# Kernel tuning notes

Measured on AMD Instinct MI355X. Metric: run time of the kernel, lower is better.

The kernel has to match this reference:

```python
import jax, jax.numpy as jnp
import numpy as np

VERTICES = np.array([[-1.0, -1.0, 1.0], [-1.0, 1.0, 1.0], [1.0, 1.0, 1.0], [1.0, -1.0, 1.0]], dtype=np.float32)  # [4,3]


def _gather2d(img, yi, xi):
    # img: [C,IH,IW], yi/xi: [OH,OW] int32 -> [C,OH,OW]
    return img[:, yi, xi]


def _grid_sample_bilinear_zero(inp, grid):
    # inp: [B,C,IH,IW], grid: [B,OH,OW,2] in [-1,1] (x,y), align_corners=True (old torch semantics)
    B, C, IH, IW = inp.shape
    gx = grid[..., 0]
    gy = grid[..., 1]
    ix = (gx + 1.0) * (IW - 1) * 0.5
    iy = (gy + 1.0) * (IH - 1) * 0.5
    x0 = jnp.floor(ix)
    y0 = jnp.floor(iy)
    x1 = x0 + 1.0
    y1 = y0 + 1.0
    wx1 = ix - x0  # frac weights
    wy1 = iy - y0
    wx0 = 1.0 - wx1
    wy0 = 1.0 - wy1

    def corner(xf, yf, w):
        inb = ((xf >= 0) & (xf <= IW - 1) & (yf >= 0) & (yf <= IH - 1)).astype(inp.dtype)
        xi = jnp.clip(xf, 0, IW - 1).astype(jnp.int32)
        yi = jnp.clip(yf, 0, IH - 1).astype(jnp.int32)
        vals = jax.vmap(_gather2d)(inp, yi, xi)  # [B,C,OH,OW]
        return vals * (w * inb)[:, None, :, :]

    out = (corner(x0, y0, wx0 * wy0) + corner(x1, y0, wx1 * wy0)
           + corner(x0, y1, wx0 * wy1) + corner(x1, y1, wx1 * wy1))
    return out


def affine_spatial_transform(inp, theta, OH, OW):
    B, C, IH, IW = inp.shape
    hs = jnp.linspace(-1.0, 1.0, OH)
    ws = jnp.linspace(-1.0, 1.0, OW)
    hh = jnp.broadcast_to(hs[:, None], (OH, OW))
    ww = jnp.broadcast_to(ws[None, :], (OH, OW))
    t = jnp.stack([ww, hh, jnp.ones((OH, OW), dtype=inp.dtype)], axis=2)  # [OH,OW,3]
    # source_grid = theta @ t : [B,OH,OW,2]
    grid = jnp.einsum('bij,hwj->bhwi', theta, t)
    out = _grid_sample_bilinear_zero(inp, grid)
    v = jnp.asarray(VERTICES)  # [4,3]
    vout = jnp.einsum('bij,vj->bvi', theta, v)  # [B,4,2]
    x_coord = (vout[..., 0] + 1.0) * IW * 0.5
    y_coord = (vout[..., 1] + 1.0) * IH * 0.5
    vertices_out = jnp.stack([x_coord, y_coord], axis=2)  # [B,4,2]
    return out, vertices_out


def setup_inputs() -> dict:
    key = jax.random.key(0)
    k1, k2 = jax.random.split(key)
    B, C, IH, IW = 16, 64, 256, 256
    inp = jax.random.normal(k1, (B, C, IH, IW), dtype=jnp.float32)
    theta = jax.random.normal(k2, (B, 2, 3), dtype=jnp.float32)
    return {"input": inp, "theta": theta, "OH": 256, "OW": 256}


def reference(input, theta, OH, OW):
    return affine_spatial_transform(input, theta, OH, OW)
```

## Files before the change

kernel.cpp:

```cpp
#include <hip/hip_runtime.h>

#define B  16
#define C  64
#define IH 256
#define IW 256
#define OH 256
#define OW 256

#define TW 16
#define TH 16
#define NWT (OW / TW)
#define NHT (OH / TH)
#define NB  (B * NHT * NWT)
#define CAP 4096

typedef float f4 __attribute__((ext_vector_type(4)));
typedef float f2 __attribute__((ext_vector_type(2)));
typedef f2 __attribute__((aligned(4))) f2u;

__global__ __launch_bounds__(256) void ast_fused(const float* __restrict__ inp,
                                                 const float* __restrict__ theta,
                                                 float* __restrict__ out) {
    const int tid = threadIdx.x;

    if (blockIdx.x == 0 && tid < B * 4) {
        const int b_ = tid >> 2;
        const int v  = tid & 3;
        const float vx_tab[4] = {-1.0f, -1.0f, 1.0f, 1.0f};
        const float vy_tab[4] = {-1.0f,  1.0f, 1.0f, -1.0f};
        const float Vx = vx_tab[v];
        const float Vy = vy_tab[v];
        const float ox = theta[b_*6+0]*Vx + theta[b_*6+1]*Vy + theta[b_*6+2];
        const float oy = theta[b_*6+3]*Vx + theta[b_*6+4]*Vy + theta[b_*6+5];
        float* vo = out + (size_t)B * C * OH * OW;
        vo[b_*8 + v*2 + 0] = (ox + 1.0f) * ((float)IW * 0.5f);
        vo[b_*8 + v*2 + 1] = (oy + 1.0f) * ((float)IH * 0.5f);
    }

    int id = (int)blockIdx.x;
    id = (id & 7) * (NB >> 3) + (id >> 3);

    const int wt = id & (NWT - 1);
    const int ht = (id >> 4) & (NHT - 1);
    const int b  = id >> 8;

    const int tx = tid & (TW - 1);
    const int ty = tid >> 4;
    const int w = wt * TW + tx;
    const int h = ht * TH + ty;

    const float t00 = theta[b*6+0], t01 = theta[b*6+1], t02 = theta[b*6+2];
    const float t10 = theta[b*6+3], t11 = theta[b*6+4], t12 = theta[b*6+5];

    const float sWn = 2.0f / (float)(OW - 1);
    const float sHn = 2.0f / (float)(OH - 1);

    const float wn = -1.0f + sWn * (float)w;
    const float hn = -1.0f + sHn * (float)h;
    const float ix = (t00 * wn + t01 * hn + t02 + 1.0f) * ((float)(IW - 1) * 0.5f);
    const float iy = (t10 * wn + t11 * hn + t12 + 1.0f) * ((float)(IH - 1) * 0.5f);

    const float x0f = floorf(ix);
    const float y0f = floorf(iy);
    const float wx1 = ix - x0f;
    const float wy1 = iy - y0f;
    const float wx0 = 1.0f - wx1;
    const float wy0 = 1.0f - wy1;

    const bool inx0 = (x0f >= 0.0f) && (x0f <= (float)(IW - 1));
    const bool inx1 = (x0f + 1.0f >= 0.0f) && (x0f + 1.0f <= (float)(IW - 1));
    const bool iny0 = (y0f >= 0.0f) && (y0f <= (float)(IH - 1));
    const bool iny1 = (y0f + 1.0f >= 0.0f) && (y0f + 1.0f <= (float)(IH - 1));

    const float w00 = (inx0 && iny0) ? wx0 * wy0 : 0.0f;
    const float w10 = (inx1 && iny0) ? wx1 * wy0 : 0.0f;
    const float w01 = (inx0 && iny1) ? wx0 * wy1 : 0.0f;
    const float w11 = (inx1 && iny1) ? wx1 * wy1 : 0.0f;

    const float wnA = -1.0f + sWn * (float)(wt * TW);
    const float wnB = -1.0f + sWn * (float)(wt * TW + TW - 1);
    const float hnA = -1.0f + sHn * (float)(ht * TH);
    const float hnB = -1.0f + sHn * (float)(ht * TH + TH - 1);

    const float ixAA = (t00*wnA + t01*hnA + t02 + 1.0f) * 127.5f;
    const float ixAB = (t00*wnA + t01*hnB + t02 + 1.0f) * 127.5f;
    const float ixBA = (t00*wnB + t01*hnA + t02 + 1.0f) * 127.5f;
    const float ixBB = (t00*wnB + t01*hnB + t02 + 1.0f) * 127.5f;
    const float iyAA = (t10*wnA + t11*hnA + t12 + 1.0f) * 127.5f;
    const float iyAB = (t10*wnA + t11*hnB + t12 + 1.0f) * 127.5f;
    const float iyBA = (t10*wnB + t11*hnA + t12 + 1.0f) * 127.5f;
    const float iyBB = (t10*wnB + t11*hnB + t12 + 1.0f) * 127.5f;

    const float min_ix = fminf(fminf(ixAA, ixAB), fminf(ixBA, ixBB));
    const float max_ix = fmaxf(fmaxf(ixAA, ixAB), fmaxf(ixBA, ixBB));
    const float min_iy = fminf(fminf(iyAA, iyAB), fminf(iyBA, iyBB));
    const float max_iy = fmaxf(fmaxf(iyAA, iyAB), fmaxf(iyBA, iyBB));

    float* o = out + ((size_t)(b * C) << 16) + (size_t)(h * OW + w);

    if (max_ix < -1.0f || min_ix > 256.0f || max_iy < -1.0f || min_iy > 256.0f) {
        #pragma unroll 8
        for (int c = 0; c < C; ++c) {
            __builtin_nontemporal_store(0.0f, o);
            o += OH * OW;
        }
        return;
    }

    const int bx0 = min(max((int)floorf(min_ix) - 1, 0), IW - 1);
    const int bx1 = min(max((int)floorf(max_ix) + 2, 0), IW - 1);
    const int by0 = min(max((int)floorf(min_iy) - 1, 0), IH - 1);
    const int by1 = min(max((int)floorf(max_iy) + 2, 0), IH - 1);

    const int Wneed = bx1 - bx0 + 4;
    int lw = 32 - __builtin_clz((unsigned)(Wneed - 1));
    if (lw < 3) lw = 3;
    if (lw > 8) lw = 8;
    const int P   = 1 << lw;
    const int Pp  = P + 4;
    const int ax0p = min(bx0 & ~3, IW - P);
    const int Hd  = by1 - by0 + 1;

    const int x0i = (int)x0f;
    const int y0i = (int)y0f;
    const float* plane = inp + ((size_t)(b * C) << 16);

    if (Hd * Pp > CAP) {
        const int  basex = min(max(x0i, 0), IW - 2);
        const bool sA = (x0i <= IW - 2);
        const bool sB = (x0i >= 0);
        const int  y0c = min(max(y0i,     0), IH - 1);
        const int  y1c = min(max(y0i + 1, 0), IH - 1);
        const int off0 = y0c * IW + basex;
        const int off1 = y1c * IW + basex;
        const float* pl = plane;
        for (int c = 0; c < C; ++c) {
            const f2 ra = *(const f2u*)(pl + off0);
            const f2 rb = *(const f2u*)(pl + off1);
            const float a00 = sA ? ra.x : ra.y;
            const float a10 = sB ? ra.y : ra.x;
            const float b00 = sA ? rb.x : rb.y;
            const float b11 = sB ? rb.y : rb.x;
            float v = w00 * a00;
            v = fmaf(w10, a10, v);
            v = fmaf(w01, b00, v);
            v = fmaf(w11, b11, v);
            __builtin_nontemporal_store(v, o);
            pl += IH * IW;
            o  += OH * OW;
        }
        return;
    }

    const int xin = x0i - ax0p;
    const int rin = y0i - by0;
    const int xc0 = min(max(xin, 0), P - 2);
    const bool selA = (xin <= P - 2);
    const bool selB = (xin >= 0);
    const int r0 = min(max(rin,     0), Hd - 1);
    const int r1 = min(max(rin + 1, 0), Hd - 1);
    const int ad0 = r0 * Pp + xc0;
    const int ad1 = r1 * Pp + xc0;

    const int S = Hd << lw;
    int  gsrc[4];
    int  ldst[4];
    bool act[4];
    #pragma unroll
    for (int g = 0; g < 4; ++g) {
        const int i4 = g * 1024 + (tid << 2);
        act[g] = (i4 < S);
        const int r  = i4 >> lw;
        const int xb = i4 & (P - 1);
        gsrc[g] = (by0 + r) * IW + ax0p + xb;
        ldst[g] = r * Pp + xb;
    }

    __shared__ float sb[2][CAP];

    f4 pf[4];
    #pragma unroll
    for (int g = 0; g < 4; ++g)
        if (act[g]) pf[g] = *(const f4*)(plane + gsrc[g]);

    #pragma unroll 2
    for (int c = 0; c < C; ++c) {
        const int cur = c & 1;
        float* dst = &sb[cur][0];
        #pragma unroll
        for (int g = 0; g < 4; ++g)
            if (act[g]) *(f4*)(dst + ldst[g]) = pf[g];
        if (c + 1 < C) {
            const float* pl = plane + ((size_t)(c + 1) << 16);
            #pragma unroll
            for (int g = 0; g < 4; ++g)
                if (act[g]) pf[g] = *(const f4*)(pl + gsrc[g]);
        }
        __syncthreads();
        const float* Lb = &sb[cur][0];
        const float p00 = Lb[ad0], p01 = Lb[ad0 + 1];
        const float p10 = Lb[ad1], p11 = Lb[ad1 + 1];
        const float a00 = selA ? p00 : p01;
        const float a10 = selB ? p01 : p00;
        const float b00 = selA ? p10 : p11;
        const float b11 = selB ? p11 : p10;
        float v = w00 * a00;
        v = fmaf(w10, a10, v);
        v = fmaf(w01, b00, v);
        v = fmaf(w11, b11, v);
        __builtin_nontemporal_store(v, o);
        o += OH * OW;
    }
}

extern "C" void kernel_launch(void* const* d_in, const int* in_sizes, int n_in,
                              void* d_out, int out_size, void* d_ws, size_t ws_size,
                              hipStream_t stream) {
    const float* inp   = (const float*)d_in[0];
    const float* theta = (const float*)d_in[1];
    float* out = (float*)d_out;

    ast_fused<<<NB, 256, 0, stream>>>(inp, theta, out);
}
```

Before: 579.9 us.

## Shrink LDS tile, deepen channel prefetch pipeline, use lightweight barriers

```diff
diff --git a/kernel.cpp b/kernel.cpp
--- a/kernel.cpp
+++ b/kernel.cpp
@@ -12,15 +12,22 @@
 #define NWT (OW / TW)
 #define NHT (OH / TH)
 #define NB  (B * NHT * NWT)
-#define CAP 4096
+#define CAPU 2048
+#define CAPF (CAPU + 256)
 
 typedef float f4 __attribute__((ext_vector_type(4)));
 typedef float f2 __attribute__((ext_vector_type(2)));
 typedef f2 __attribute__((aligned(4))) f2u;
 
-__global__ __launch_bounds__(256) void ast_fused(const float* __restrict__ inp,
-                                                 const float* __restrict__ theta,
-                                                 float* __restrict__ out) {
+#define BAR() do {                                         \
+    asm volatile("s_waitcnt lgkmcnt(0)" ::: "memory");     \
+    __builtin_amdgcn_s_barrier();                          \
+    asm volatile("" ::: "memory");                         \
+} while (0)
+
+__global__ __launch_bounds__(256, 8) void ast_fused(const float* __restrict__ inp,
+                                                    const float* __restrict__ theta,
+                                                    float* __restrict__ out) {
     const int tid = threadIdx.x;
 
     if (blockIdx.x == 0 && tid < B * 4) {
@@ -116,16 +123,16 @@
     int lw = 32 - __builtin_clz((unsigned)(Wneed - 1));
     if (lw < 3) lw = 3;
     if (lw > 8) lw = 8;
-    const int P   = 1 << lw;
-    const int Pp  = P + 4;
+    const int P    = 1 << lw;
+    const int Pp   = P + 4;
     const int ax0p = min(bx0 & ~3, IW - P);
-    const int Hd  = by1 - by0 + 1;
+    const int Hd   = by1 - by0 + 1;
 
     const int x0i = (int)x0f;
     const int y0i = (int)y0f;
     const float* plane = inp + ((size_t)(b * C) << 16);
 
-    if (Hd * Pp > CAP) {
+    if (Hd * Pp > CAPU) {
         const int  basex = min(max(x0i, 0), IW - 2);
         const bool sA = (x0i <= IW - 2);
         const bool sB = (x0i >= 0);
@@ -163,54 +170,83 @@
     const int ad1 = r1 * Pp + xc0;
 
     const int S = Hd << lw;
-    int  gsrc[4];
-    int  ldst[4];
-    bool act[4];
+    int gsrc[2], ldst[2];
     #pragma unroll
-    for (int g = 0; g < 4; ++g) {
+    for (int g = 0; g < 2; ++g) {
         const int i4 = g * 1024 + (tid << 2);
-        act[g] = (i4 < S);
-        const int r  = i4 >> lw;
-        const int xb = i4 & (P - 1);
-        gsrc[g] = (by0 + r) * IW + ax0p + xb;
-        ldst[g] = r * Pp + xb;
-    }
-
-    __shared__ float sb[2][CAP];
-
-    f4 pf[4];
-    #pragma unroll
-    for (int g = 0; g < 4; ++g)
-        if (act[g]) pf[g] = *(const f4*)(plane + gsrc[g]);
-
-    #pragma unroll 2
-    for (int c = 0; c < C; ++c) {
-        const int cur = c & 1;
-        float* dst = &sb[cur][0];
-        #pragma unroll
-        for (int g = 0; g < 4; ++g)
-            if (act[g]) *(f4*)(dst + ldst[g]) = pf[g];
-        if (c + 1 < C) {
-            const float* pl = plane + ((size_t)(c + 1) << 16);
-            #pragma unroll
-            for (int g = 0; g < 4; ++g)
-                if (act[g]) pf[g] = *(const f4*)(pl + gsrc[g]);
+        if (i4 < S) {
+            const int r  = i4 >> lw;
+            const int xb = i4 & (P - 1);
+            gsrc[g] = (by0 + r) * IW + ax0p + xb;
+            ldst[g] = r * Pp + xb;
+        } else {
+            gsrc[g] = by0 * IW + ax0p;
+            ldst[g] = CAPU + ((tid & 63) << 2);
         }
-        __syncthreads();
-        const float* Lb = &sb[cur][0];
+    }
+
+    __shared__ float sb[2][CAPF];
+    float* const b0 = &sb[0][0];
+    float* const b1 = &sb[1][0];
+
+    auto samp = [&](const float* Lb) -> float {
         const float p00 = Lb[ad0], p01 = Lb[ad0 + 1];
         const float p10 = Lb[ad1], p11 = Lb[ad1 + 1];
         const float a00 = selA ? p00 : p01;
         const float a10 = selB ? p01 : p00;
-        const float b00 = selA ? p10 : p11;
-        const float b11 = selB ? p11 : p10;
+        const float c00 = selA ? p10 : p11;
+        const float c11 = selB ? p11 : p10;
         float v = w00 * a00;
         v = fmaf(w10, a10, v);
-        v = fmaf(w01, b00, v);
-        v = fmaf(w11, b11, v);
-        __builtin_nontemporal_store(v, o);
+        v = fmaf(w01, c00, v);
+        v = fmaf(w11, c11, v);
+        return v;
+    };
+
+    const float* pld = plane;
+    f4 pfA0, pfA1, pfB0, pfB1;
+
+    pfA0 = *(const f4*)(pld + gsrc[0]);
+    pfA1 = *(const f4*)(pld + gsrc[1]);
+    pld += IH * IW;
+    pfB0 = *(const f4*)(pld + gsrc[0]);
+    pfB1 = *(const f4*)(pld + gsrc[1]);
+    pld += IH * IW;
+    *(f4*)(b0 + ldst[0]) = pfA0;
+    *(f4*)(b0 + ldst[1]) = pfA1;
+    BAR();
+
+    #pragma unroll 1
+    for (int k = 0; k < 31; ++k) {
+        pfA0 = *(const f4*)(pld + gsrc[0]);
+        pfA1 = *(const f4*)(pld + gsrc[1]);
+        pld += IH * IW;
+        *(f4*)(b1 + ldst[0]) = pfB0;
+        *(f4*)(b1 + ldst[1]) = pfB1;
+        const float v0 = samp(b0);
+        BAR();
+        __builtin_nontemporal_store(v0, o);
         o += OH * OW;
-    }
+
+        pfB0 = *(const f4*)(pld + gsrc[0]);
+        pfB1 = *(const f4*)(pld + gsrc[1]);
+        pld += IH * IW;
+        *(f4*)(b0 + ldst[0]) = pfA0;
+        *(f4*)(b0 + ldst[1]) = pfA1;
+        const float v1 = samp(b1);
+        BAR();
+        __builtin_nontemporal_store(v1, o);
+        o += OH * OW;
+    }
+
+    *(f4*)(b1 + ldst[0]) = pfB0;
+    *(f4*)(b1 + ldst[1]) = pfB1;
+    const float v62 = samp(b0);
+    BAR();
+    __builtin_nontemporal_store(v62, o);
+    o += OH * OW;
+    const float v63 = samp(b1);
+    __builtin_nontemporal_store(v63, o);
 }
 
 extern "C" void kernel_launch(void* const* d_in, const int* in_sizes, int n_in,
```

After: 529.5 us. 8.7% less time.
